# Kernel optimization log

Hardware: AMD Instinct MI355X
Metric: run time of the kernel (lower is better)

Reference implementation:

```python
import jax, jax.numpy as jnp
import numpy as np


def setup_inputs() -> dict:
    key = jax.random.key(0)
    k1, k2, k3, k4 = jax.random.split(key, 4)
    batch, n_channels, t = 4, 2048, 2048
    n_blocks, block_size, ks = 128, 64, 16
    n_block_row = n_channels // block_size  # 32
    x = jax.random.normal(k1, (batch, n_channels, t), dtype=jnp.float32)
    block_values = jax.random.normal(k2, (n_blocks, block_size, block_size, ks), dtype=jnp.float32) * 0.05
    cols = jax.random.randint(k3, (n_blocks,), 0, n_block_row, dtype=jnp.int32)
    rows = jax.random.randint(k4, (n_blocks,), 0, n_block_row, dtype=jnp.int32)
    return {"x": x, "block_values": block_values, "cols": cols, "rows": rows}


def reference(x, block_values, cols, rows):
    # x: (B, C, T); block_values: (n_blocks, bs, bs, ks)
    batch, n_channels, t = x.shape
    n_blocks, bs, _, ks = block_values.shape
    n_block_row = -(-n_channels // bs)
    pad = n_block_row * bs - n_channels
    if pad > 0:
        x = jnp.pad(x, ((0, 0), (0, pad), (0, 0)))
    xb = x.reshape(batch, n_block_row, bs, t)
    # gather active block rows: (B, n_blocks, bs, T) -> (B, n_blocks*bs, T)
    x_unfold = xb[:, cols].reshape(batch, n_blocks * bs, t)
    # grouped causal conv: weights shared across batch, groups = n_blocks
    W = block_values.reshape(n_blocks * bs, bs, ks)  # (O, I/g, K)
    o = jax.lax.conv_general_dilated(
        x_unfold, W,
        window_strides=(1,),
        padding=[(ks - 1, 0)],  # causal: equals padding=ks-1 then [..., :t]
        dimension_numbers=("NCH", "OIH", "NCH"),
        feature_group_count=n_blocks,
    )  # (B, n_blocks*bs, T)
    o = o.reshape(batch, n_blocks, bs, t)
    # scatter-add block outputs into their target block rows
    y = jnp.zeros((batch, n_block_row, bs, t), o.dtype).at[:, rows].add(o)
    y = y.reshape(batch, n_block_row * bs, t)
    return y[:, :n_channels, :]
```

## Files before the change

### kernel.cpp

```cpp
#include <hip/hip_runtime.h>
#include <hip/hip_bf16.h>
#include <stdint.h>

typedef __bf16 bf16_t;
typedef bf16_t bf16x8 __attribute__((ext_vector_type(8)));
typedef float f32x4 __attribute__((ext_vector_type(4)));

#define T_LEN 2048
#define C_LEN 2048
#define NB 128
#define TN 256
#define SROWS 2064
#define XROWS 288

#define GLL(gp, lp) __builtin_amdgcn_global_load_lds( \
    (const __attribute__((address_space(1))) uint32_t*)(gp), \
    (__attribute__((address_space(3))) uint32_t*)(lp), 16, 0, 0)

__global__ __launch_bounds__(256) void prepack_kernel(
    const float* __restrict__ bv, bf16_t* __restrict__ wpk)
{
  const int blk = blockIdx.x;
  const int mt  = blockIdx.y;
  const int tid = threadIdx.x;
  __shared__ float lw[16 * 64 * 17];

  const float* src = bv + (size_t)blk * 65536 + (size_t)mt * 16384;
  for (int p = 0; p < 16; ++p) {
    int idx = p * 1024 + tid * 4;
    const float4 v = *(const float4*)(src + idx);
    int o = idx >> 10;
    int i = (idx >> 4) & 63;
    int k = idx & 15;
    float* d = &lw[(o * 64 + i) * 17 + k];
    d[0] = v.x; d[1] = v.y; d[2] = v.z; d[3] = v.w;
  }
  __syncthreads();

  const int e0 = tid * 2;
  const int l  = e0 >> 3;
  const int j  = e0 & 7;
  const int o  = l & 15;
  for (int ks = 0; ks < 32; ++ks) {
    const int k  = ks >> 1;
    const int i0 = (ks & 1) * 32 + (l >> 4) * 8 + j;
    const float a = lw[(o * 64 + i0) * 17 + k];
    const float b = lw[(o * 64 + i0 + 1) * 17 + k];
    const uint16_t ba = __builtin_bit_cast(uint16_t, (bf16_t)a);
    const uint16_t bb = __builtin_bit_cast(uint16_t, (bf16_t)b);
    const uint32_t packed = (uint32_t)ba | ((uint32_t)bb << 16);
    const size_t off = ((((size_t)blk * 32 + ks) * 4 + mt) * 512) + e0;
    *(uint32_t*)(wpk + off) = packed;
  }
}

__global__ __launch_bounds__(256) void padzero_kernel(bf16_t* __restrict__ S)
{
  const int p = blockIdx.x;
  const size_t g = (p < 64) ? ((size_t)(p >> 4) * SROWS + (p & 15))
                            : ((size_t)4 * SROWS + (p - 64));
  uint4 z = {0u, 0u, 0u, 0u};
  *(uint4*)(S + g * C_LEN + (size_t)threadIdx.x * 8) = z;
}

__global__ __launch_bounds__(256) void xprep_kernel(
    const float* __restrict__ x, bf16_t* __restrict__ S)
{
  const int tb = blockIdx.x, cb = blockIdx.y, n = blockIdx.z;
  const int tid = threadIdx.x;
  __shared__ float lt[64 * 67 + 4];

  #pragma unroll
  for (int p = 0; p < 4; ++p) {
    const int idx = p * 256 + tid;
    const int c   = idx >> 4;
    const int t4  = (idx & 15) * 4;
    const float4 v = *(const float4*)(
        x + ((size_t)n * C_LEN + cb * 64 + c) * T_LEN + tb * 64 + t4);
    float* d = &lt[c * 67 + t4];
    d[0] = v.x; d[1] = v.y; d[2] = v.z; d[3] = v.w;
  }
  __syncthreads();

  #pragma unroll
  for (int p = 0; p < 2; ++p) {
    const int idx = p * 256 + tid;
    const int tl  = idx >> 3;
    const int seg = idx & 7;
    const int t   = tb * 64 + tl;
    const int cbase = (seg * 8) ^ ((t & 7) << 3);
    uint32_t w[4];
    #pragma unroll
    for (int h = 0; h < 4; ++h) {
      const float a = lt[(cbase + 2 * h) * 67 + tl];
      const float b = lt[(cbase + 2 * h + 1) * 67 + tl];
      const uint16_t ba = __builtin_bit_cast(uint16_t, (bf16_t)a);
      const uint16_t bb = __builtin_bit_cast(uint16_t, (bf16_t)b);
      w[h] = (uint32_t)ba | ((uint32_t)bb << 16);
    }
    uint4 u4 = {w[0], w[1], w[2], w[3]};
    *(uint4*)(S + ((size_t)n * SROWS + 16 + t) * C_LEN + cb * 64 + seg * 8) = u4;
  }
}

__global__ __launch_bounds__(256, 2) void bsconv_kernel(
    const bf16_t* __restrict__ S, const bf16_t* __restrict__ wpk,
    const int* __restrict__ cols, const int* __restrict__ rows,
    float* __restrict__ y)
{
  const int tt = blockIdx.x, tr = blockIdx.y, n = blockIdx.z;
  const int t0 = tt * TN;
  const int tid = threadIdx.x;
  const int lane = tid & 63, wv = tid >> 6;

  __shared__ __attribute__((aligned(16))) bf16_t xst[XROWS * 64];
  __shared__ __attribute__((aligned(16))) bf16_t wlds[2][8192];
  __shared__ int alist[NB];
  __shared__ int clds[NB];
  __shared__ unsigned long long wmask[2];

  {
    const int r = (tid < NB) ? rows[tid] : -1;
    if (tid < NB) clds[tid] = cols[tid];
    const bool match = (r == tr);
    const unsigned long long m = __ballot(match);
    if (wv < 2 && lane == 0) wmask[wv] = m;
    __syncthreads();
    if (match) {
      int pos = __popcll(wmask[wv] & ((1ull << lane) - 1ull));
      if (wv == 1) pos += __popcll(wmask[0]);
      alist[pos] = tid;
    }
    __syncthreads();
  }
  const int cnt = __popcll(wmask[0]) + __popcll(wmask[1]);

  f32x4 acc[4][4];
  #pragma unroll
  for (int a = 0; a < 4; ++a)
    #pragma unroll
    for (int b = 0; b < 4; ++b) {
      f32x4 z = {0.f, 0.f, 0.f, 0.f};
      acc[a][b] = z;
    }

  const size_t srow0 = (size_t)n * SROWS + t0;
  const int lxb = tid * 16;

  auto issue_x = [&](int cb) {
    #pragma unroll
    for (int q = 0; q < 9; ++q) {
      const int lb = q * 4096 + lxb;
      const int u  = lb >> 7;
      const int ib = (lb >> 1) & 63;
      GLL(S + (srow0 + u) * C_LEN + cb * 64 + ib, (char*)xst + lb);
    }
  };
  auto issue_w = [&](const bf16_t* wsrc, int buf) {
    #pragma unroll
    for (int p = 0; p < 4; ++p) {
      const int lb = p * 4096 + lxb;
      GLL(wsrc + (lb >> 1), (char*)wlds[buf] + lb);
    }
  };

  if (cnt > 0) {
    issue_x(clds[alist[0]]);
    issue_w(wpk + (size_t)alist[0] * 65536, 0);
  }

  for (int j = 0; j < cnt; ++j) {
    const bf16_t* wblk = wpk + (size_t)alist[j] * 65536;
    const bool havenext = (j + 1 < cnt);
    const int bnext = havenext ? alist[j + 1] : 0;

    #pragma unroll
    for (int c = 0; c < 8; ++c) {
      if (c < 7) {
        issue_w(wblk + (size_t)(c + 1) * 8192, (c + 1) & 1);
      } else if (havenext) {
        issue_w(wpk + (size_t)bnext * 65536, 0);
      }

      if (c < 7 || havenext) {
        asm volatile("s_waitcnt vmcnt(4)" ::: "memory");
      } else {
        asm volatile("s_waitcnt vmcnt(0)" ::: "memory");
      }
      __builtin_amdgcn_s_barrier();
      __builtin_amdgcn_sched_barrier(0);

      const bf16_t* wl = wlds[c & 1];
      __builtin_amdgcn_s_setprio(1);
      #pragma unroll
      for (int ksl = 0; ksl < 4; ++ksl) {
        const int ks = c * 4 + ksl;
        const int k  = ks >> 1;
        const int ih = (ks & 1) * 32;
        bf16x8 afr[4];
        #pragma unroll
        for (int mt = 0; mt < 4; ++mt)
          afr[mt] = *(const bf16x8*)(wl + ((ksl * 4 + mt) * 64 + lane) * 8);
        const int ub   = wv * 64 + (lane & 15) + k + 1;
        const int scol = (ih + ((lane >> 4) & 3) * 8) ^ ((ub & 7) << 3);
        bf16x8 bfr[4];
        #pragma unroll
        for (int nt = 0; nt < 4; ++nt)
          bfr[nt] = *(const bf16x8*)(xst + (ub + nt * 16) * 64 + scol);
        #pragma unroll
        for (int mt = 0; mt < 4; ++mt)
          #pragma unroll
          for (int nt = 0; nt < 4; ++nt)
            acc[mt][nt] = __builtin_amdgcn_mfma_f32_16x16x32_bf16(
                afr[mt], bfr[nt], acc[mt][nt], 0, 0, 0);
      }
      __builtin_amdgcn_s_setprio(0);
      __builtin_amdgcn_sched_barrier(0);
      __builtin_amdgcn_s_barrier();
    }

    if (havenext) issue_x(clds[bnext]);
  }

  const int mlo = ((lane >> 4) & 3) * 4, nn = lane & 15;
  #pragma unroll
  for (int mt = 0; mt < 4; ++mt) {
    #pragma unroll
    for (int nt = 0; nt < 4; ++nt) {
      const int t = t0 + wv * 64 + nt * 16 + nn;
      float* yp = y + ((size_t)n * C_LEN + (size_t)(tr * 64 + mt * 16 + mlo)) * T_LEN + t;
      #pragma unroll
      for (int r = 0; r < 4; ++r)
        yp[(size_t)r * T_LEN] = acc[mt][nt][r];
    }
  }
}

extern "C" void kernel_launch(void* const* d_in, const int* in_sizes, int n_in,
                              void* d_out, int out_size, void* d_ws, size_t ws_size,
                              hipStream_t stream) {
  const float* x   = (const float*)d_in[0];
  const float* bv  = (const float*)d_in[1];
  const int* cols  = (const int*)d_in[2];
  const int* rows  = (const int*)d_in[3];
  float* y = (float*)d_out;

  bf16_t* wpk = (bf16_t*)d_ws;
  bf16_t* S   = (bf16_t*)((char*)d_ws + 16777216);

  prepack_kernel<<<dim3(128, 4), dim3(256), 0, stream>>>(bv, wpk);
  padzero_kernel<<<dim3(80), dim3(256), 0, stream>>>(S);
  xprep_kernel<<<dim3(32, 32, 4), dim3(256), 0, stream>>>(x, S);
  bsconv_kernel<<<dim3(8, 32, 4), dim3(256), 0, stream>>>(S, wpk, cols, rows, y);
}
```

Baseline: 175.7 us.

## Pipeline weight chunks through a 5-slot LDS ring with register-prefetched fragments

```diff
diff --git a/kernel.cpp b/kernel.cpp
--- a/kernel.cpp
+++ b/kernel.cpp
@@ -114,14 +114,13 @@
   const int lane = tid & 63, wv = tid >> 6;
 
   __shared__ __attribute__((aligned(16))) bf16_t xst[XROWS * 64];
-  __shared__ __attribute__((aligned(16))) bf16_t wlds[2][8192];
+  __shared__ __attribute__((aligned(16))) bf16_t wring[5][4096];
   __shared__ int alist[NB];
-  __shared__ int clds[NB];
   __shared__ unsigned long long wmask[2];
 
   {
-    const int r = (tid < NB) ? rows[tid] : -1;
-    if (tid < NB) clds[tid] = cols[tid];
+    const int r  = (tid < NB) ? rows[tid] : -1;
+    const int cb = (tid < NB) ? cols[tid] : 0;
     const bool match = (r == tr);
     const unsigned long long m = __ballot(match);
     if (wv < 2 && lane == 0) wmask[wv] = m;
@@ -129,7 +128,7 @@
     if (match) {
       int pos = __popcll(wmask[wv] & ((1ull << lane) - 1ull));
       if (wv == 1) pos += __popcll(wmask[0]);
-      alist[pos] = tid;
+      alist[pos] = tid | (cb << 8);
     }
     __syncthreads();
   }
@@ -156,70 +155,69 @@
       GLL(S + (srow0 + u) * C_LEN + cb * 64 + ib, (char*)xst + lb);
     }
   };
-  auto issue_w = [&](const bf16_t* wsrc, int buf) {
-    #pragma unroll
-    for (int p = 0; p < 4; ++p) {
+  auto issue_wc = [&](const bf16_t* wblk, int c, int slot) {
+    const bf16_t* wsrc = wblk + (size_t)c * 4096;
+    #pragma unroll
+    for (int p = 0; p < 2; ++p) {
       const int lb = p * 4096 + lxb;
-      GLL(wsrc + (lb >> 1), (char*)wlds[buf] + lb);
+      GLL(wsrc + (lb >> 1), (char*)wring[slot] + lb);
     }
   };
 
-  if (cnt > 0) {
-    issue_x(clds[alist[0]]);
-    issue_w(wpk + (size_t)alist[0] * 65536, 0);
-  }
+  bf16x8 afr[2][4], bfr[2][4];
+  auto read_frags = [&](int c) {
+    const bf16_t* wl = wring[c % 5];
+    #pragma unroll
+    for (int kk = 0; kk < 2; ++kk) {
+      #pragma unroll
+      for (int mt = 0; mt < 4; ++mt)
+        afr[kk][mt] = *(const bf16x8*)(wl + ((kk * 4 + mt) * 64 + lane) * 8);
+      const int ub   = wv * 64 + (lane & 15) + c + 1;
+      const int scol = (kk * 32 + ((lane >> 4) & 3) * 8) ^ ((ub & 7) << 3);
+      #pragma unroll
+      for (int nt = 0; nt < 4; ++nt)
+        bfr[kk][nt] = *(const bf16x8*)(xst + (ub + nt * 16) * 64 + scol);
+    }
+  };
 
   for (int j = 0; j < cnt; ++j) {
-    const bf16_t* wblk = wpk + (size_t)alist[j] * 65536;
-    const bool havenext = (j + 1 < cnt);
-    const int bnext = havenext ? alist[j + 1] : 0;
-
-    #pragma unroll
-    for (int c = 0; c < 8; ++c) {
-      if (c < 7) {
-        issue_w(wblk + (size_t)(c + 1) * 8192, (c + 1) & 1);
-      } else if (havenext) {
-        issue_w(wpk + (size_t)bnext * 65536, 0);
-      }
-
-      if (c < 7 || havenext) {
-        asm volatile("s_waitcnt vmcnt(4)" ::: "memory");
-      } else {
-        asm volatile("s_waitcnt vmcnt(0)" ::: "memory");
-      }
-      __builtin_amdgcn_s_barrier();
+    const int aj = alist[j];
+    const bf16_t* wblk = wpk + (size_t)(aj & 255) * 65536;
+    const int cb = aj >> 8;
+
+    issue_x(cb);
+    issue_wc(wblk, 0, 0);
+    issue_wc(wblk, 1, 1);
+    issue_wc(wblk, 2, 2);
+    issue_wc(wblk, 3, 3);
+    asm volatile("s_waitcnt vmcnt(4)" ::: "memory");
+    __builtin_amdgcn_s_barrier();
+    read_frags(0);
+
+    for (int c = 0; c < 16; ++c) {
+      asm volatile("s_waitcnt lgkmcnt(0)" ::: "memory");
       __builtin_amdgcn_sched_barrier(0);
-
-      const bf16_t* wl = wlds[c & 1];
+      if (c <= 11) issue_wc(wblk, c + 4, (c + 4) % 5);
       __builtin_amdgcn_s_setprio(1);
       #pragma unroll
-      for (int ksl = 0; ksl < 4; ++ksl) {
-        const int ks = c * 4 + ksl;
-        const int k  = ks >> 1;
-        const int ih = (ks & 1) * 32;
-        bf16x8 afr[4];
-        #pragma unroll
-        for (int mt = 0; mt < 4; ++mt)
-          afr[mt] = *(const bf16x8*)(wl + ((ksl * 4 + mt) * 64 + lane) * 8);
-        const int ub   = wv * 64 + (lane & 15) + k + 1;
-        const int scol = (ih + ((lane >> 4) & 3) * 8) ^ ((ub & 7) << 3);
-        bf16x8 bfr[4];
-        #pragma unroll
-        for (int nt = 0; nt < 4; ++nt)
-          bfr[nt] = *(const bf16x8*)(xst + (ub + nt * 16) * 64 + scol);
+      for (int kk = 0; kk < 2; ++kk)
         #pragma unroll
         for (int mt = 0; mt < 4; ++mt)
           #pragma unroll
           for (int nt = 0; nt < 4; ++nt)
             acc[mt][nt] = __builtin_amdgcn_mfma_f32_16x16x32_bf16(
-                afr[mt], bfr[nt], acc[mt][nt], 0, 0, 0);
-      }
+                afr[kk][mt], bfr[kk][nt], acc[mt][nt], 0, 0, 0);
       __builtin_amdgcn_s_setprio(0);
       __builtin_amdgcn_sched_barrier(0);
+      if (c < 15) {
+        if (c <= 11)      asm volatile("s_waitcnt vmcnt(4)" ::: "memory");
+        else if (c == 12) asm volatile("s_waitcnt vmcnt(2)" ::: "memory");
+        else              asm volatile("s_waitcnt vmcnt(0)" ::: "memory");
+        read_frags(c + 1);
+        __builtin_amdgcn_sched_barrier(0);
+      }
       __builtin_amdgcn_s_barrier();
     }
-
-    if (havenext) issue_x(clds[bnext]);
   }
 
   const int mlo = ((lane >> 4) & 3) * 4, nn = lane & 15;
```

After: 175.6 us. No clear change (-0.0%).
